# Kernel tuning notes

Measured on AMD Instinct MI355X. Metric: run time of the kernel, lower is better.

## Reference

```python
import jax, jax.numpy as jnp
import numpy as np

B, L, H = 16, 4096, 768

def setup_inputs() -> dict:
    key = jax.random.key(0)
    k1, k2 = jax.random.split(key)
    sequence_output = jax.random.normal(k1, (B, L, H), dtype=jnp.float32)
    # sorted segment ids: each wordpiece position maps to a token index in [0, L)
    wordpiece_to_token = jnp.sort(
        jax.random.randint(k2, (B, L), 0, L, dtype=jnp.int32), axis=-1)
    return {"sequence_output": sequence_output,
            "wordpiece_to_token": wordpiece_to_token}

def reference(sequence_output, wordpiece_to_token):
    # For each (batch, token j): output[b, j] = sum of sequence_output[b, p]
    # over wordpieces p assigned to token j. Tokens with no wordpieces stay 0,
    # matching torch.zeros_like initialization in the original.
    num_tokens = sequence_output.shape[1]
    def per_example(x, seg):  # x: [L, H], seg: [L]
        return jax.ops.segment_sum(x, seg, num_segments=num_tokens)
    return jax.vmap(per_example)(sequence_output, wordpiece_to_token)
```

## Files before the change

kernel.cpp:

```cpp
#include <hip/hip_runtime.h>

#define BB 16
#define LL 4096
#define HH 768
#define H4 (HH / 4)

__global__ __launch_bounds__(256) void boundaries_kernel(
    const int* __restrict__ seg, int* __restrict__ start) {
    int idx = blockIdx.x * blockDim.x + threadIdx.x;
    if (idx >= BB * (LL + 1)) return;
    int b = idx / (LL + 1);
    int p = idx - b * (LL + 1);
    const int* s = seg + (size_t)b * LL;
    int cur  = (p < LL) ? s[p]     : LL;
    int prev = (p > 0)  ? s[p - 1] : -1;
    int* st = start + (size_t)b * (LL + 1);
    for (int j = prev + 1; j <= cur; ++j) st[j] = p;
}

__global__ __launch_bounds__(256) void segsum_kernel(
    const float4* __restrict__ x, const int* __restrict__ start,
    float4* __restrict__ out) {
    int gtid = blockIdx.x * blockDim.x + threadIdx.x;
    int wave = gtid >> 6;
    int lane = gtid & 63;
    int b = wave >> 12;
    int j = wave & (LL - 1);

    const int* st = start + (size_t)b * (LL + 1) + j;
    int s = st[0];
    int e = st[1];

    float4 a0 = make_float4(0.f, 0.f, 0.f, 0.f);
    float4 a1 = a0, a2 = a0;

    const float4* xb = x + (size_t)b * LL * H4;
    for (int p = s; p < e; ++p) {
        const float4* row = xb + (size_t)p * H4 + lane;
        float4 v0 = row[0];
        float4 v1 = row[64];
        float4 v2 = row[128];
        a0.x += v0.x; a0.y += v0.y; a0.z += v0.z; a0.w += v0.w;
        a1.x += v1.x; a1.y += v1.y; a1.z += v1.z; a1.w += v1.w;
        a2.x += v2.x; a2.y += v2.y; a2.z += v2.z; a2.w += v2.w;
    }

    float4* orow = out + (size_t)wave * H4 + lane;
    orow[0]   = a0;
    orow[64]  = a1;
    orow[128] = a2;
}

extern "C" void kernel_launch(void* const* d_in, const int* in_sizes, int n_in,
                              void* d_out, int out_size, void* d_ws, size_t ws_size,
                              hipStream_t stream) {
    const float* x   = (const float*)d_in[0];
    const int*   seg = (const int*)d_in[1];
    float* out = (float*)d_out;
    int* start = (int*)d_ws;

    int nb_threads = BB * (LL + 1);
    boundaries_kernel<<<(nb_threads + 255) / 256, 256, 0, stream>>>(seg, start);

    int nblocks = (BB * LL) / 4;
    segsum_kernel<<<nblocks, 256, 0, stream>>>(
        (const float4*)x, start, (float4*)out);
}
```

Baseline: 334.8 us.

## Fuse boundary computation into segsum via two-level wave ballot search

```diff
diff --git a/kernel.cpp b/kernel.cpp
--- a/kernel.cpp
+++ b/kernel.cpp
@@ -2,24 +2,10 @@
 
 #define BB 16
 #define LL 4096
-#define HH 768
-#define H4 (HH / 4)
+#define H4 192
 
-__global__ __launch_bounds__(256) void boundaries_kernel(
-    const int* __restrict__ seg, int* __restrict__ start) {
-    int idx = blockIdx.x * blockDim.x + threadIdx.x;
-    if (idx >= BB * (LL + 1)) return;
-    int b = idx / (LL + 1);
-    int p = idx - b * (LL + 1);
-    const int* s = seg + (size_t)b * LL;
-    int cur  = (p < LL) ? s[p]     : LL;
-    int prev = (p > 0)  ? s[p - 1] : -1;
-    int* st = start + (size_t)b * (LL + 1);
-    for (int j = prev + 1; j <= cur; ++j) st[j] = p;
-}
-
-__global__ __launch_bounds__(256) void segsum_kernel(
-    const float4* __restrict__ x, const int* __restrict__ start,
+__global__ __launch_bounds__(256) void segsum_fused_kernel(
+    const float4* __restrict__ x, const int* __restrict__ seg,
     float4* __restrict__ out) {
     int gtid = blockIdx.x * blockDim.x + threadIdx.x;
     int wave = gtid >> 6;
@@ -27,9 +13,33 @@
     int b = wave >> 12;
     int j = wave & (LL - 1);
 
-    const int* st = start + (size_t)b * (LL + 1) + j;
-    int s = st[0];
-    int e = st[1];
+    const int* __restrict__ sb = seg + ((size_t)b << 12);
+
+    int v1 = sb[lane << 6];
+    unsigned long long ms = __ballot(v1 >= j);
+    unsigned long long me = __ballot(v1 > j);
+
+    int s, e;
+    if (ms & 1ull) {
+        s = 0;
+    } else {
+        int f = ms ? (__ffsll((unsigned long long)ms) - 1) : 64;
+        int base = ((f - 1) << 6) + 1;
+        int p2 = base + lane;
+        int v2 = (p2 < LL) ? sb[p2] : 0x7fffffff;
+        unsigned long long m2 = __ballot(v2 >= j);
+        s = base + __ffsll(m2) - 1;
+    }
+    if (me & 1ull) {
+        e = 0;
+    } else {
+        int f = me ? (__ffsll((unsigned long long)me) - 1) : 64;
+        int base = ((f - 1) << 6) + 1;
+        int p2 = base + lane;
+        int v2 = (p2 < LL) ? sb[p2] : 0x7fffffff;
+        unsigned long long m2 = __ballot(v2 > j);
+        e = base + __ffsll(m2) - 1;
+    }
 
     float4 a0 = make_float4(0.f, 0.f, 0.f, 0.f);
     float4 a1 = a0, a2 = a0;
@@ -38,11 +48,11 @@
     for (int p = s; p < e; ++p) {
         const float4* row = xb + (size_t)p * H4 + lane;
         float4 v0 = row[0];
-        float4 v1 = row[64];
-        float4 v2 = row[128];
+        float4 vA = row[64];
+        float4 vB = row[128];
         a0.x += v0.x; a0.y += v0.y; a0.z += v0.z; a0.w += v0.w;
-        a1.x += v1.x; a1.y += v1.y; a1.z += v1.z; a1.w += v1.w;
-        a2.x += v2.x; a2.y += v2.y; a2.z += v2.z; a2.w += v2.w;
+        a1.x += vA.x; a1.y += vA.y; a1.z += vA.z; a1.w += vA.w;
+        a2.x += vB.x; a2.y += vB.y; a2.z += vB.z; a2.w += vB.w;
     }
 
     float4* orow = out + (size_t)wave * H4 + lane;
@@ -57,12 +67,9 @@
     const float* x   = (const float*)d_in[0];
     const int*   seg = (const int*)d_in[1];
     float* out = (float*)d_out;
-    int* start = (int*)d_ws;
-
-    int nb_threads = BB * (LL + 1);
-    boundaries_kernel<<<(nb_threads + 255) / 256, 256, 0, stream>>>(seg, start);
+    (void)d_ws; (void)ws_size;
 
     int nblocks = (BB * LL) / 4;
-    segsum_kernel<<<nblocks, 256, 0, stream>>>(
-        (const float4*)x, start, (float4*)out);
+    segsum_fused_kernel<<<nblocks, 256, 0, stream>>>(
+        (const float4*)x, seg, (float4*)out);
 }
```

After: 328.9 us. Within noise of the previous version (-1.8%).
